# Kernel optimization log

Hardware: AMD Instinct MI355X
Metric: run time of the kernel (lower is better)

## Reference

```python
import jax, jax.numpy as jnp
import numpy as np

B, OUT, IN = 4096, 1024, 1024
BN_EPS = 1e-5


def setup_inputs() -> dict:
    key = jax.random.key(0)
    kx, k1, k2, k3 = jax.random.split(key, 4)
    # kaiming_uniform_ with a=sqrt(5): bound = sqrt(6 / ((1+a^2) * fan_in)) = 1/sqrt(fan_in)
    bound = 1.0 / np.sqrt(IN)
    x = jax.random.normal(kx, (B, IN), dtype=jnp.float32)
    c1 = jax.random.uniform(k1, (OUT, IN), jnp.float32, -bound, bound)
    c2 = jax.random.uniform(k2, (OUT, IN), jnp.float32, -bound, bound)
    c3 = jax.random.uniform(k3, (OUT, IN), jnp.float32, -bound, bound)
    bias = jnp.zeros((OUT, IN), jnp.float32)
    gamma = jnp.ones((OUT,), jnp.float32)   # BatchNorm1d weight
    beta = jnp.zeros((OUT,), jnp.float32)   # BatchNorm1d bias
    return {"x": x, "c1": c1, "c2": c2, "c3": c3, "bias": bias,
            "gamma": gamma, "beta": beta}


def reference(x, c1, c2, c3, bias, gamma, beta):
    # Fused polynomial 'matmul': out[b,o] = sum_i x*c1 + x^2*c2 + x^3*c3 + bias
    x2 = x * x
    x3 = x2 * x
    y = (jnp.einsum('bi,oi->bo', x, c1)
         + jnp.einsum('bi,oi->bo', x2, c2)
         + jnp.einsum('bi,oi->bo', x3, c3)
         + jnp.sum(bias, axis=1))  # bias reduced over in_features
    # BatchNorm1d (training mode: batch statistics, biased variance)
    mean = jnp.mean(y, axis=0)
    var = jnp.var(y, axis=0)
    return (y - mean) * jax.lax.rsqrt(var + BN_EPS) * gamma + beta
```

## Files before the change

### kernel.cpp

```cpp
#include <hip/hip_runtime.h>
#include <stdint.h>

#define B_ROWS 4096
#define OUTF   1024
#define INF    1024
#define KTOT   3072
#define BN_EPS 1e-5f
#define BM 128
#define BN 128
#define BK 64
#define NSTEP (KTOT / BK)

typedef short  short8  __attribute__((ext_vector_type(8)));
typedef float  floatx4 __attribute__((ext_vector_type(4)));

struct alignas(8) s4 { short x, y, z, w; };

#define WAIT_VM4 0x0F74
#define WAIT_VM2 0x0F72
#define WAIT_VM0 0x0F70

__device__ __forceinline__ short f2bf(float f) {
  union { float f; uint32_t u; } cv; cv.f = f;
  uint32_t u = cv.u;
  uint32_t r = (u + 0x7fffu + ((u >> 16) & 1u)) >> 16;
  return (short)r;
}

__device__ __forceinline__ void load_lds16(const void* g, void* l) {
  __builtin_amdgcn_global_load_lds(
      (const __attribute__((address_space(1))) uint32_t*)(uintptr_t)g,
      (__attribute__((address_space(3))) uint32_t*)(uint32_t)(uintptr_t)l,
      16, 0, 0);
}

__global__ void prep_all(const float4* __restrict__ x4,
                         const float4* __restrict__ c1, const float4* __restrict__ c2,
                         const float4* __restrict__ c3,
                         short* __restrict__ Xb, short* __restrict__ Wb) {
  int b = blockIdx.x;
  if (b < 4096) {
    int idx = b * 256 + threadIdx.x;
    float4 v = x4[idx];
    int row = idx >> 8;
    int c   = (idx & 255) << 2;
    size_t base = (size_t)row * KTOT + c;
    s4 p1 = { f2bf(v.x), f2bf(v.y), f2bf(v.z), f2bf(v.w) };
    float ax = v.x * v.x, ay = v.y * v.y, az = v.z * v.z, aw = v.w * v.w;
    s4 p2 = { f2bf(ax), f2bf(ay), f2bf(az), f2bf(aw) };
    s4 p3 = { f2bf(ax * v.x), f2bf(ay * v.y), f2bf(az * v.z), f2bf(aw * v.w) };
    *(s4*)&Xb[base]        = p1;
    *(s4*)&Xb[base + 1024] = p2;
    *(s4*)&Xb[base + 2048] = p3;
  } else {
    int idx = (b - 4096) * 256 + threadIdx.x;
    int row = idx >> 8;
    int c   = (idx & 255) << 2;
    size_t base = (size_t)row * KTOT + c;
    float4 a = c1[idx], bb = c2[idx], d = c3[idx];
    s4 p1 = { f2bf(a.x),  f2bf(a.y),  f2bf(a.z),  f2bf(a.w)  };
    s4 p2 = { f2bf(bb.x), f2bf(bb.y), f2bf(bb.z), f2bf(bb.w) };
    s4 p3 = { f2bf(d.x),  f2bf(d.y),  f2bf(d.z),  f2bf(d.w)  };
    *(s4*)&Wb[base]        = p1;
    *(s4*)&Wb[base + 1024] = p2;
    *(s4*)&Wb[base + 2048] = p3;
  }
}

__global__ __launch_bounds__(1024, 4) void gemm_poly(
    const short* __restrict__ Xb, const short* __restrict__ Wb,
    float* __restrict__ Y, float* __restrict__ psum, float* __restrict__ psq) {
  __shared__ __align__(16) short As[4][BM * BK];
  __shared__ __align__(16) short Bs[4][BN * BK];
  const int tid  = threadIdx.x;
  const int lane = tid & 63;
  const int wave = tid >> 6;
  const int wr = wave >> 2;
  const int wc = wave & 3;
  const int lb  = blockIdx.x;
  const int xcd = lb & 7;
  const int sl  = lb >> 3;
  const int bx  = sl & 7;
  const int by  = xcd * 4 + (sl >> 3);
  const int row0 = by * BM;
  const int col0 = bx * BN;
  const short* Ag = Xb + (size_t)row0 * KTOT;
  const short* Bg = Wb + (size_t)col0 * KTOT;
  const int frag_m = lane & 15;
  const int sel = lane >> 4;
  floatx4 acc[2][2] = {};

  const int soff = (tid >> 3) * KTOT + ((tid & 7) ^ ((tid >> 3) & 7)) * 8;
  const int ldst = tid * 8;

  #pragma unroll
  for (int t = 0; t < 3; ++t) {
    load_lds16(Ag + soff + t * BK, &As[t][ldst]);
    load_lds16(Bg + soff + t * BK, &Bs[t][ldst]);
  }

#define GSTEP(CUR, PRE, KT_PRE, DO_PRE, WAITIMM)                              \
  {                                                                           \
    __builtin_amdgcn_s_waitcnt(WAITIMM);                                      \
    __builtin_amdgcn_s_barrier();                                             \
    if (DO_PRE) {                                                             \
      load_lds16(Ag + soff + (KT_PRE), &As[PRE][ldst]);                       \
      load_lds16(Bg + soff + (KT_PRE), &Bs[PRE][ldst]);                       \
    }                                                                         \
    _Pragma("unroll")                                                         \
    for (int s = 0; s < 2; ++s) {                                             \
      short8 af[2], bfr[2];                                                   \
      _Pragma("unroll")                                                       \
      for (int i = 0; i < 2; ++i) {                                           \
        int r = wr * 32 + i * 16 + frag_m;                                    \
        int p = (s * 4 + sel) ^ (r & 7);                                      \
        af[i] = *(const short8*)&As[CUR][r * BK + p * 8];                     \
      }                                                                       \
      _Pragma("unroll")                                                       \
      for (int j = 0; j < 2; ++j) {                                           \
        int r = wc * 32 + j * 16 + frag_m;                                    \
        int p = (s * 4 + sel) ^ (r & 7);                                      \
        bfr[j] = *(const short8*)&Bs[CUR][r * BK + p * 8];                    \
      }                                                                       \
      _Pragma("unroll")                                                       \
      for (int i = 0; i < 2; ++i)                                             \
        _Pragma("unroll")                                                     \
        for (int j = 0; j < 2; ++j)                                           \
          acc[i][j] = __builtin_amdgcn_mfma_f32_16x16x32_bf16(                \
              af[i], bfr[j], acc[i][j], 0, 0, 0);                             \
    }                                                                         \
  }

  for (int t4 = 0; t4 < 44; t4 += 4) {
    GSTEP(0, 3, (t4 + 3) * BK, 1, WAIT_VM4);
    GSTEP(1, 0, (t4 + 4) * BK, 1, WAIT_VM4);
    GSTEP(2, 1, (t4 + 5) * BK, 1, WAIT_VM4);
    GSTEP(3, 2, (t4 + 6) * BK, 1, WAIT_VM4);
  }
  GSTEP(0, 3, 47 * BK, 1, WAIT_VM4);
  GSTEP(1, 0, 0, 0, WAIT_VM4);
  GSTEP(2, 0, 0, 0, WAIT_VM2);
  GSTEP(3, 0, 0, 0, WAIT_VM0);
#undef GSTEP

  float* colred = (float*)&As[0][0];
  float sv[2] = {0.f, 0.f}, sq[2] = {0.f, 0.f};
  #pragma unroll
  for (int j = 0; j < 2; ++j)
    #pragma unroll
    for (int i = 0; i < 2; ++i)
      #pragma unroll
      for (int r = 0; r < 4; ++r) {
        float v = acc[i][j][r];
        sv[j] += v; sq[j] += v * v;
      }
  #pragma unroll
  for (int j = 0; j < 2; ++j) {
    sv[j] += __shfl_xor(sv[j], 16, 64); sv[j] += __shfl_xor(sv[j], 32, 64);
    sq[j] += __shfl_xor(sq[j], 16, 64); sq[j] += __shfl_xor(sq[j], 32, 64);
  }
  if (sel == 0) {
    #pragma unroll
    for (int j = 0; j < 2; ++j) {
      int cc = wc * 32 + j * 16 + frag_m;
      colred[(wr * 2 + 0) * 128 + cc] = sv[j];
      colred[(wr * 2 + 1) * 128 + cc] = sq[j];
    }
  }
  #pragma unroll
  for (int j = 0; j < 2; ++j) {
    int gc = col0 + wc * 32 + j * 16 + frag_m;
    #pragma unroll
    for (int i = 0; i < 2; ++i) {
      int gr = row0 + wr * 32 + i * 16 + sel * 4;
      #pragma unroll
      for (int r = 0; r < 4; ++r)
        Y[(size_t)(gr + r) * OUTF + gc] = acc[i][j][r];
    }
  }
  __syncthreads();
  if (tid < BN) {
    float s0 = colred[0 * 128 + tid] + colred[2 * 128 + tid]
             + colred[4 * 128 + tid] + colred[6 * 128 + tid];
    float s1 = colred[1 * 128 + tid] + colred[3 * 128 + tid]
             + colred[5 * 128 + tid] + colred[7 * 128 + tid];
    psum[(size_t)by * OUTF + col0 + tid] = s0;
    psq [(size_t)by * OUTF + col0 + tid] = s1;
  }
}

__global__ void bn_fused(const float* __restrict__ psum, const float* __restrict__ psq,
                         const float* __restrict__ gamma, const float* __restrict__ beta,
                         float* __restrict__ Y) {
  __shared__ float sc[32], sh[32];
  const int c0 = blockIdx.x * 32;
  const int t = threadIdx.x;
  if (t < 32) {
    float s = 0.f, s2 = 0.f;
    #pragma unroll 8
    for (int p = 0; p < 32; ++p) {
      s  += psum[p * OUTF + c0 + t];
      s2 += psq [p * OUTF + c0 + t];
    }
    float mean = s * (1.0f / B_ROWS);
    float var  = s2 * (1.0f / B_ROWS) - mean * mean;
    float scale = gamma[c0 + t] * rsqrtf(var + BN_EPS);
    sc[t] = scale;
    sh[t] = beta[c0 + t] - mean * scale;
  }
  __syncthreads();
  const int f4c = t & 7;
  const int rr  = t >> 3;
  const int row0 = blockIdx.y * 256;
  float4* Y4 = (float4*)Y;
  const int cb = f4c * 4;
  float s0 = sc[cb], s1 = sc[cb+1], s2 = sc[cb+2], s3 = sc[cb+3];
  float h0 = sh[cb], h1 = sh[cb+1], h2 = sh[cb+2], h3 = sh[cb+3];
  #pragma unroll
  for (int it = 0; it < 8; ++it) {
    int row = row0 + it * 32 + rr;
    size_t idx = (size_t)row * 256 + (c0 >> 2) + f4c;
    float4 v = Y4[idx];
    v.x = v.x * s0 + h0; v.y = v.y * s1 + h1;
    v.z = v.z * s2 + h2; v.w = v.w * s3 + h3;
    Y4[idx] = v;
  }
}

extern "C" void kernel_launch(void* const* d_in, const int* in_sizes, int n_in,
                              void* d_out, int out_size, void* d_ws, size_t ws_size,
                              hipStream_t stream) {
  const float* x     = (const float*)d_in[0];
  const float* c1    = (const float*)d_in[1];
  const float* c2    = (const float*)d_in[2];
  const float* c3    = (const float*)d_in[3];
  const float* gamma = (const float*)d_in[5];
  const float* beta  = (const float*)d_in[6];
  float* out = (float*)d_out;
  char* ws = (char*)d_ws;

  short* Xb   = (short*)(ws);
  short* Wb   = (short*)(ws + 25165824);
  float* psum = (float*)(ws + 31457280);
  float* psq  = (float*)(ws + 31588352);

  prep_all<<<5120, 256, 0, stream>>>((const float4*)x, (const float4*)c1,
                                     (const float4*)c2, (const float4*)c3,
                                     Xb, Wb);

  gemm_poly<<<256, 1024, 0, stream>>>(Xb, Wb, out, psum, psq);

  dim3 bgrid(OUTF / 32, B_ROWS / 256);
  bn_fused<<<bgrid, 256, 0, stream>>>(psum, psq, gamma, beta, out);
}
```

Baseline: 123.7 us.

## Use 256-thread blocks with 64x64 per-wave tiles in polynomial GEMM

Shrinks the GEMM workgroup from 16 waves to 4 waves, so each wave now computes a 64x64 sub-tile (4x4 MFMA fragments) instead of 32x32. The intent is more register-level operand reuse per LDS fragment read and cheaper barriers. Each thread now issues four global-to-LDS loads per operand per stage, and the vmcnt wait immediates are adjusted to match. The cost is fewer waves per CU to hide latency, since only 256 blocks of 4 waves run on the device, and higher register pressure.

```diff
diff --git a/kernel.cpp b/kernel.cpp
--- a/kernel.cpp
+++ b/kernel.cpp
@@ -16,9 +16,9 @@
 
 struct alignas(8) s4 { short x, y, z, w; };
 
-#define WAIT_VM4 0x0F74
-#define WAIT_VM2 0x0F72
-#define WAIT_VM0 0x0F70
+#define WAIT_VM16 0x4F70
+#define WAIT_VM8  0x0F78
+#define WAIT_VM0  0x0F70
 
 __device__ __forceinline__ short f2bf(float f) {
   union { float f; uint32_t u; } cv; cv.f = f;
@@ -67,7 +67,7 @@
   }
 }
 
-__global__ __launch_bounds__(1024, 4) void gemm_poly(
+__global__ __launch_bounds__(256, 1) void gemm_poly(
     const short* __restrict__ Xb, const short* __restrict__ Wb,
     float* __restrict__ Y, float* __restrict__ psum, float* __restrict__ psq) {
   __shared__ __align__(16) short As[4][BM * BK];
@@ -75,8 +75,8 @@
   const int tid  = threadIdx.x;
   const int lane = tid & 63;
   const int wave = tid >> 6;
-  const int wr = wave >> 2;
-  const int wc = wave & 3;
+  const int wr = wave >> 1;
+  const int wc = wave & 1;
   const int lb  = blockIdx.x;
   const int xcd = lb & 7;
   const int sl  = lb >> 3;
@@ -88,15 +88,24 @@
   const short* Bg = Wb + (size_t)col0 * KTOT;
   const int frag_m = lane & 15;
   const int sel = lane >> 4;
-  floatx4 acc[2][2] = {};
-
-  const int soff = (tid >> 3) * KTOT + ((tid & 7) ^ ((tid >> 3) & 7)) * 8;
-  const int ldst = tid * 8;
+  floatx4 acc[4][4] = {};
+
+  int soff[4], ldst[4];
+  #pragma unroll
+  for (int q = 0; q < 4; ++q) {
+    int c = tid + q * 256;
+    soff[q] = (c >> 3) * KTOT + ((c & 7) ^ ((c >> 3) & 7)) * 8;
+    ldst[q] = c * 8;
+  }
 
   #pragma unroll
   for (int t = 0; t < 3; ++t) {
-    load_lds16(Ag + soff + t * BK, &As[t][ldst]);
-    load_lds16(Bg + soff + t * BK, &Bs[t][ldst]);
+    #pragma unroll
+    for (int q = 0; q < 4; ++q)
+      load_lds16(Ag + soff[q] + t * BK, &As[t][ldst[q]]);
+    #pragma unroll
+    for (int q = 0; q < 4; ++q)
+      load_lds16(Bg + soff[q] + t * BK, &Bs[t][ldst[q]]);
   }
 
 #define GSTEP(CUR, PRE, KT_PRE, DO_PRE, WAITIMM)                              \
@@ -104,75 +113,79 @@
     __builtin_amdgcn_s_waitcnt(WAITIMM);                                      \
     __builtin_amdgcn_s_barrier();                                             \
     if (DO_PRE) {                                                             \
-      load_lds16(Ag + soff + (KT_PRE), &As[PRE][ldst]);                       \
-      load_lds16(Bg + soff + (KT_PRE), &Bs[PRE][ldst]);                       \
+      _Pragma("unroll")                                                       \
+      for (int q = 0; q < 4; ++q)                                             \
+        load_lds16(Ag + soff[q] + (KT_PRE), &As[PRE][ldst[q]]);               \
+      _Pragma("unroll")                                                       \
+      for (int q = 0; q < 4; ++q)                                             \
+        load_lds16(Bg + soff[q] + (KT_PRE), &Bs[PRE][ldst[q]]);               \
     }                                                                         \
     _Pragma("unroll")                                                         \
     for (int s = 0; s < 2; ++s) {                                             \
-      short8 af[2], bfr[2];                                                   \
-      _Pragma("unroll")                                                       \
-      for (int i = 0; i < 2; ++i) {                                           \
-        int r = wr * 32 + i * 16 + frag_m;                                    \
+      short8 af[4], bfr[4];                                                   \
+      _Pragma("unroll")                                                       \
+      for (int i = 0; i < 4; ++i) {                                           \
+        int r = wr * 64 + i * 16 + frag_m;                                    \
         int p = (s * 4 + sel) ^ (r & 7);                                      \
         af[i] = *(const short8*)&As[CUR][r * BK + p * 8];                     \
       }                                                                       \
       _Pragma("unroll")                                                       \
-      for (int j = 0; j < 2; ++j) {                                           \
-        int r = wc * 32 + j * 16 + frag_m;                                    \
+      for (int j = 0; j < 4; ++j) {                                           \
+        int r = wc * 64 + j * 16 + frag_m;                                    \
         int p = (s * 4 + sel) ^ (r & 7);                                      \
         bfr[j] = *(const short8*)&Bs[CUR][r * BK + p * 8];                    \
       }                                                                       \
       _Pragma("unroll")                                                       \
-      for (int i = 0; i < 2; ++i)                                             \
+      for (int i = 0; i < 4; ++i)                                             \
         _Pragma("unroll")                                                     \
-        for (int j = 0; j < 2; ++j)                                           \
+        for (int j = 0; j < 4; ++j)                                           \
           acc[i][j] = __builtin_amdgcn_mfma_f32_16x16x32_bf16(                \
               af[i], bfr[j], acc[i][j], 0, 0, 0);                             \
     }                                                                         \
   }
 
   for (int t4 = 0; t4 < 44; t4 += 4) {
-    GSTEP(0, 3, (t4 + 3) * BK, 1, WAIT_VM4);
-    GSTEP(1, 0, (t4 + 4) * BK, 1, WAIT_VM4);
-    GSTEP(2, 1, (t4 + 5) * BK, 1, WAIT_VM4);
-    GSTEP(3, 2, (t4 + 6) * BK, 1, WAIT_VM4);
-  }
-  GSTEP(0, 3, 47 * BK, 1, WAIT_VM4);
-  GSTEP(1, 0, 0, 0, WAIT_VM4);
-  GSTEP(2, 0, 0, 0, WAIT_VM2);
+    GSTEP(0, 3, (t4 + 3) * BK, 1, WAIT_VM16);
+    GSTEP(1, 0, (t4 + 4) * BK, 1, WAIT_VM16);
+    GSTEP(2, 1, (t4 + 5) * BK, 1, WAIT_VM16);
+    GSTEP(3, 2, (t4 + 6) * BK, 1, WAIT_VM16);
+  }
+  GSTEP(0, 3, 47 * BK, 1, WAIT_VM16);
+  GSTEP(1, 0, 0, 0, WAIT_VM16);
+  GSTEP(2, 0, 0, 0, WAIT_VM8);
   GSTEP(3, 0, 0, 0, WAIT_VM0);
 #undef GSTEP
 
   float* colred = (float*)&As[0][0];
-  float sv[2] = {0.f, 0.f}, sq[2] = {0.f, 0.f};
-  #pragma unroll
-  for (int j = 0; j < 2; ++j)
-    #pragma unroll
-    for (int i = 0; i < 2; ++i)
+  float sv[4] = {0.f, 0.f, 0.f, 0.f}, sq[4] = {0.f, 0.f, 0.f, 0.f};
+  #pragma unroll
+  for (int j = 0; j < 4; ++j)
+    #pragma unroll
+    for (int i = 0; i < 4; ++i)
       #pragma unroll
       for (int r = 0; r < 4; ++r) {
         float v = acc[i][j][r];
         sv[j] += v; sq[j] += v * v;
       }
   #pragma unroll
-  for (int j = 0; j < 2; ++j) {
+  for (int j = 0; j < 4; ++j) {
     sv[j] += __shfl_xor(sv[j], 16, 64); sv[j] += __shfl_xor(sv[j], 32, 64);
     sq[j] += __shfl_xor(sq[j], 16, 64); sq[j] += __shfl_xor(sq[j], 32, 64);
   }
   if (sel == 0) {
     #pragma unroll
-    for (int j = 0; j < 2; ++j) {
-      int cc = wc * 32 + j * 16 + frag_m;
+    for (int j = 0; j < 4; ++j) {
+      int cc = wc * 64 + j * 16 + frag_m;
       colred[(wr * 2 + 0) * 128 + cc] = sv[j];
       colred[(wr * 2 + 1) * 128 + cc] = sq[j];
     }
   }
   #pragma unroll
-  for (int j = 0; j < 2; ++j) {
-    int gc = col0 + wc * 32 + j * 16 + frag_m;
-    #pragma unroll
-    for (int i = 0; i < 2; ++i) {
-      int gr = row0 + wr * 32 + i * 16 + sel * 4;
+  for (int j = 0; j < 4; ++j) {
+    int gc = col0 + wc * 64 + j * 16 + frag_m;
+    #pragma unroll
+    for (int i = 0; i < 4; ++i) {
+      int gr = row0 + wr * 64 + i * 16 + sel * 4;
       #pragma unroll
       for (int r = 0; r < 4; ++r)
         Y[(size_t)(gr + r) * OUTF + gc] = acc[i][j][r];
@@ -180,10 +193,8 @@
   }
   __syncthreads();
   if (tid < BN) {
-    float s0 = colred[0 * 128 + tid] + colred[2 * 128 + tid]
-             + colred[4 * 128 + tid] + colred[6 * 128 + tid];
-    float s1 = colred[1 * 128 + tid] + colred[3 * 128 + tid]
-             + colred[5 * 128 + tid] + colred[7 * 128 + tid];
+    float s0 = colred[0 * 128 + tid] + colred[2 * 128 + tid];
+    float s1 = colred[1 * 128 + tid] + colred[3 * 128 + tid];
     psum[(size_t)by * OUTF + col0 + tid] = s0;
     psq [(size_t)by * OUTF + col0 + tid] = s1;
   }
@@ -248,7 +259,7 @@
                                      (const float4*)c2, (const float4*)c3,
                                      Xb, Wb);
 
-  gemm_poly<<<256, 1024, 0, stream>>>(Xb, Wb, out, psum, psq);
+  gemm_poly<<<256, 256, 0, stream>>>(Xb, Wb, out, psum, psq);
 
   dim3 bgrid(OUTF / 32, B_ROWS / 256);
   bn_fused<<<bgrid, 256, 0, stream>>>(psum, psq, gamma, beta, out);
```

Measured after the change: 126.7 us. +2.4%, slower.

## Fuse batch-norm into GEMM epilogue via cooperative grid sync and atomics

Applied to the files above, without the earlier changes.

Removes the separate BN kernel. Each GEMM block atomically adds its column partial sums to global totals, which the prep kernel now zeroes. A cooperative grid sync follows, after which every block computes scale and shift and writes the normalized output once. This avoids writing Y and then reading and rewriting it, and drops one launch, at the cost of a grid-wide barrier and atomic contention.

```diff
diff --git a/kernel.cpp b/kernel.cpp
--- a/kernel.cpp
+++ b/kernel.cpp
@@ -1,5 +1,8 @@
 #include <hip/hip_runtime.h>
+#include <hip/hip_cooperative_groups.h>
 #include <stdint.h>
+
+namespace cg = cooperative_groups;
 
 #define B_ROWS 4096
 #define OUTF   1024
@@ -37,7 +40,8 @@
 __global__ void prep_all(const float4* __restrict__ x4,
                          const float4* __restrict__ c1, const float4* __restrict__ c2,
                          const float4* __restrict__ c3,
-                         short* __restrict__ Xb, short* __restrict__ Wb) {
+                         short* __restrict__ Xb, short* __restrict__ Wb,
+                         float* __restrict__ psz) {
   int b = blockIdx.x;
   if (b < 4096) {
     int idx = b * 256 + threadIdx.x;
@@ -52,7 +56,7 @@
     *(s4*)&Xb[base]        = p1;
     *(s4*)&Xb[base + 1024] = p2;
     *(s4*)&Xb[base + 2048] = p3;
-  } else {
+  } else if (b < 5120) {
     int idx = (b - 4096) * 256 + threadIdx.x;
     int row = idx >> 8;
     int c   = (idx & 255) << 2;
@@ -64,12 +68,17 @@
     *(s4*)&Wb[base]        = p1;
     *(s4*)&Wb[base + 1024] = p2;
     *(s4*)&Wb[base + 2048] = p3;
+  } else {
+    #pragma unroll
+    for (int k = 0; k < 8; ++k)
+      psz[threadIdx.x + k * 256] = 0.f;
   }
 }
 
 __global__ __launch_bounds__(1024, 4) void gemm_poly(
     const short* __restrict__ Xb, const short* __restrict__ Wb,
-    float* __restrict__ Y, float* __restrict__ psum, float* __restrict__ psq) {
+    float* __restrict__ Y, float* __restrict__ psumT, float* __restrict__ psqT,
+    const float* __restrict__ gamma, const float* __restrict__ beta) {
   __shared__ __align__(16) short As[4][BM * BK];
   __shared__ __align__(16) short Bs[4][BN * BK];
   const int tid  = threadIdx.x;
@@ -167,63 +176,46 @@
       colred[(wr * 2 + 1) * 128 + cc] = sq[j];
     }
   }
-  #pragma unroll
-  for (int j = 0; j < 2; ++j) {
-    int gc = col0 + wc * 32 + j * 16 + frag_m;
-    #pragma unroll
-    for (int i = 0; i < 2; ++i) {
-      int gr = row0 + wr * 32 + i * 16 + sel * 4;
-      #pragma unroll
-      for (int r = 0; r < 4; ++r)
-        Y[(size_t)(gr + r) * OUTF + gc] = acc[i][j][r];
-    }
-  }
   __syncthreads();
   if (tid < BN) {
     float s0 = colred[0 * 128 + tid] + colred[2 * 128 + tid]
              + colred[4 * 128 + tid] + colred[6 * 128 + tid];
     float s1 = colred[1 * 128 + tid] + colred[3 * 128 + tid]
              + colred[5 * 128 + tid] + colred[7 * 128 + tid];
-    psum[(size_t)by * OUTF + col0 + tid] = s0;
-    psq [(size_t)by * OUTF + col0 + tid] = s1;
-  }
-}
-
-__global__ void bn_fused(const float* __restrict__ psum, const float* __restrict__ psq,
-                         const float* __restrict__ gamma, const float* __restrict__ beta,
-                         float* __restrict__ Y) {
-  __shared__ float sc[32], sh[32];
-  const int c0 = blockIdx.x * 32;
-  const int t = threadIdx.x;
-  if (t < 32) {
-    float s = 0.f, s2 = 0.f;
-    #pragma unroll 8
-    for (int p = 0; p < 32; ++p) {
-      s  += psum[p * OUTF + c0 + t];
-      s2 += psq [p * OUTF + c0 + t];
+    atomicAdd(&psumT[col0 + tid], s0);
+    atomicAdd(&psqT [col0 + tid], s1);
+  }
+  __threadfence();
+
+  cg::this_grid().sync();
+
+  float* scaleS = (float*)&Bs[0][0];
+  float* shiftS = scaleS + 128;
+  if (tid < BN) {
+    float S  = __hip_atomic_load(&psumT[col0 + tid], __ATOMIC_RELAXED,
+                                 __HIP_MEMORY_SCOPE_AGENT);
+    float S2 = __hip_atomic_load(&psqT [col0 + tid], __ATOMIC_RELAXED,
+                                 __HIP_MEMORY_SCOPE_AGENT);
+    float mean = S * (1.0f / B_ROWS);
+    float var  = S2 * (1.0f / B_ROWS) - mean * mean;
+    float sc_  = gamma[col0 + tid] * rsqrtf(var + BN_EPS);
+    scaleS[tid] = sc_;
+    shiftS[tid] = beta[col0 + tid] - mean * sc_;
+  }
+  __syncthreads();
+  #pragma unroll
+  for (int j = 0; j < 2; ++j) {
+    int cc = wc * 32 + j * 16 + frag_m;
+    float sc_ = scaleS[cc];
+    float sh_ = shiftS[cc];
+    int gc = col0 + cc;
+    #pragma unroll
+    for (int i = 0; i < 2; ++i) {
+      int gr = row0 + wr * 32 + i * 16 + sel * 4;
+      #pragma unroll
+      for (int r = 0; r < 4; ++r)
+        Y[(size_t)(gr + r) * OUTF + gc] = acc[i][j][r] * sc_ + sh_;
     }
-    float mean = s * (1.0f / B_ROWS);
-    float var  = s2 * (1.0f / B_ROWS) - mean * mean;
-    float scale = gamma[c0 + t] * rsqrtf(var + BN_EPS);
-    sc[t] = scale;
-    sh[t] = beta[c0 + t] - mean * scale;
-  }
-  __syncthreads();
-  const int f4c = t & 7;
-  const int rr  = t >> 3;
-  const int row0 = blockIdx.y * 256;
-  float4* Y4 = (float4*)Y;
-  const int cb = f4c * 4;
-  float s0 = sc[cb], s1 = sc[cb+1], s2 = sc[cb+2], s3 = sc[cb+3];
-  float h0 = sh[cb], h1 = sh[cb+1], h2 = sh[cb+2], h3 = sh[cb+3];
-  #pragma unroll
-  for (int it = 0; it < 8; ++it) {
-    int row = row0 + it * 32 + rr;
-    size_t idx = (size_t)row * 256 + (c0 >> 2) + f4c;
-    float4 v = Y4[idx];
-    v.x = v.x * s0 + h0; v.y = v.y * s1 + h1;
-    v.z = v.z * s2 + h2; v.w = v.w * s3 + h3;
-    Y4[idx] = v;
   }
 }
 
@@ -239,17 +231,19 @@
   float* out = (float*)d_out;
   char* ws = (char*)d_ws;
 
-  short* Xb   = (short*)(ws);
-  short* Wb   = (short*)(ws + 25165824);
-  float* psum = (float*)(ws + 31457280);
-  float* psq  = (float*)(ws + 31588352);
-
-  prep_all<<<5120, 256, 0, stream>>>((const float4*)x, (const float4*)c1,
+  short* Xb    = (short*)(ws);
+  short* Wb    = (short*)(ws + 25165824);
+  float* psumT = (float*)(ws + 31457280);
+  float* psqT  = (float*)(ws + 31461376);
+
+  prep_all<<<5121, 256, 0, stream>>>((const float4*)x, (const float4*)c1,
                                      (const float4*)c2, (const float4*)c3,
-                                     Xb, Wb);
-
-  gemm_poly<<<256, 1024, 0, stream>>>(Xb, Wb, out, psum, psq);
-
-  dim3 bgrid(OUTF / 32, B_ROWS / 256);
-  bn_fused<<<bgrid, 256, 0, stream>>>(psum, psq, gamma, beta, out);
-}
+                                     Xb, Wb, psumT);
+
+  const short* XbC = Xb;
+  const short* WbC = Wb;
+  void* kargs[] = { (void*)&XbC, (void*)&WbC, (void*)&out,
+                    (void*)&psumT, (void*)&psqT,
+                    (void*)&gamma, (void*)&beta };
+  hipLaunchCooperativeKernel(gemm_poly, dim3(256), dim3(1024), kargs, 0, stream);
+}
```

After: 231.0 us. 86.7% more time.

## Fuse x power expansion and bf16 conversion into GEMM, load fp32 X tiles

Applied to the files above, without the earlier changes.

The separate prep pass that wrote x, x², x³ as bf16 into a 24MB workspace is removed. The GEMM now streams fp32 x tiles into LDS once per 64-column chunk and computes the three powers in registers, converting to bf16 before each MFMA phase. Weights are still prepacked, and the pipeline is restructured around three K-phases per x tile with a double-buffered A buffer. This cuts global traffic and one kernel's work, at the cost of extra VALU conversion inside the GEMM loop and larger fp32 LDS tiles.

```diff
diff --git a/kernel.cpp b/kernel.cpp
--- a/kernel.cpp
+++ b/kernel.cpp
@@ -1,4 +1,5 @@
 #include <hip/hip_runtime.h>
+#include <hip/hip_bf16.h>
 #include <stdint.h>
 
 #define B_ROWS 4096
@@ -9,7 +10,6 @@
 #define BM 128
 #define BN 128
 #define BK 64
-#define NSTEP (KTOT / BK)
 
 typedef short  short8  __attribute__((ext_vector_type(8)));
 typedef float  floatx4 __attribute__((ext_vector_type(4)));
@@ -18,6 +18,7 @@
 
 #define WAIT_VM4 0x0F74
 #define WAIT_VM2 0x0F72
+#define WAIT_VM1 0x0F71
 #define WAIT_VM0 0x0F70
 
 __device__ __forceinline__ short f2bf(float f) {
@@ -34,43 +35,34 @@
       16, 0, 0);
 }
 
-__global__ void prep_all(const float4* __restrict__ x4,
-                         const float4* __restrict__ c1, const float4* __restrict__ c2,
-                         const float4* __restrict__ c3,
-                         short* __restrict__ Xb, short* __restrict__ Wb) {
-  int b = blockIdx.x;
-  if (b < 4096) {
-    int idx = b * 256 + threadIdx.x;
-    float4 v = x4[idx];
-    int row = idx >> 8;
-    int c   = (idx & 255) << 2;
-    size_t base = (size_t)row * KTOT + c;
-    s4 p1 = { f2bf(v.x), f2bf(v.y), f2bf(v.z), f2bf(v.w) };
-    float ax = v.x * v.x, ay = v.y * v.y, az = v.z * v.z, aw = v.w * v.w;
-    s4 p2 = { f2bf(ax), f2bf(ay), f2bf(az), f2bf(aw) };
-    s4 p3 = { f2bf(ax * v.x), f2bf(ay * v.y), f2bf(az * v.z), f2bf(aw * v.w) };
-    *(s4*)&Xb[base]        = p1;
-    *(s4*)&Xb[base + 1024] = p2;
-    *(s4*)&Xb[base + 2048] = p3;
-  } else {
-    int idx = (b - 4096) * 256 + threadIdx.x;
-    int row = idx >> 8;
-    int c   = (idx & 255) << 2;
-    size_t base = (size_t)row * KTOT + c;
-    float4 a = c1[idx], bb = c2[idx], d = c3[idx];
-    s4 p1 = { f2bf(a.x),  f2bf(a.y),  f2bf(a.z),  f2bf(a.w)  };
-    s4 p2 = { f2bf(bb.x), f2bf(bb.y), f2bf(bb.z), f2bf(bb.w) };
-    s4 p3 = { f2bf(d.x),  f2bf(d.y),  f2bf(d.z),  f2bf(d.w)  };
-    *(s4*)&Wb[base]        = p1;
-    *(s4*)&Wb[base + 1024] = p2;
-    *(s4*)&Wb[base + 2048] = p3;
-  }
+__device__ __forceinline__ short8 cvt8(float4 a, float4 b) {
+  union { __hip_bfloat162 h[4]; short8 s; } r;
+  r.h[0] = __float22bfloat162_rn(make_float2(a.x, a.y));
+  r.h[1] = __float22bfloat162_rn(make_float2(a.z, a.w));
+  r.h[2] = __float22bfloat162_rn(make_float2(b.x, b.y));
+  r.h[3] = __float22bfloat162_rn(make_float2(b.z, b.w));
+  return r.s;
+}
+
+__global__ void prep_w(const float4* __restrict__ c1, const float4* __restrict__ c2,
+                       const float4* __restrict__ c3, short* __restrict__ Wb) {
+  int idx = blockIdx.x * 256 + threadIdx.x;
+  int row = idx >> 8;
+  int c   = (idx & 255) << 2;
+  size_t base = (size_t)row * KTOT + c;
+  float4 a = c1[idx], bb = c2[idx], d = c3[idx];
+  s4 p1 = { f2bf(a.x),  f2bf(a.y),  f2bf(a.z),  f2bf(a.w)  };
+  s4 p2 = { f2bf(bb.x), f2bf(bb.y), f2bf(bb.z), f2bf(bb.w) };
+  s4 p3 = { f2bf(d.x),  f2bf(d.y),  f2bf(d.z),  f2bf(d.w)  };
+  *(s4*)&Wb[base]        = p1;
+  *(s4*)&Wb[base + 1024] = p2;
+  *(s4*)&Wb[base + 2048] = p3;
 }
 
 __global__ __launch_bounds__(1024, 4) void gemm_poly(
-    const short* __restrict__ Xb, const short* __restrict__ Wb,
+    const float* __restrict__ X, const short* __restrict__ Wb,
     float* __restrict__ Y, float* __restrict__ psum, float* __restrict__ psq) {
-  __shared__ __align__(16) short As[4][BM * BK];
+  __shared__ __align__(16) float As32[2][BM * BK];
   __shared__ __align__(16) short Bs[4][BN * BK];
   const int tid  = threadIdx.x;
   const int lane = tid & 63;
@@ -84,43 +76,45 @@
   const int by  = xcd * 4 + (sl >> 3);
   const int row0 = by * BM;
   const int col0 = bx * BN;
-  const short* Ag = Xb + (size_t)row0 * KTOT;
+  const float* Ag = X + (size_t)row0 * INF;
   const short* Bg = Wb + (size_t)col0 * KTOT;
   const int frag_m = lane & 15;
   const int sel = lane >> 4;
   floatx4 acc[2][2] = {};
 
-  const int soff = (tid >> 3) * KTOT + ((tid & 7) ^ ((tid >> 3) & 7)) * 8;
-  const int ldst = tid * 8;
-
-  #pragma unroll
-  for (int t = 0; t < 3; ++t) {
-    load_lds16(Ag + soff + t * BK, &As[t][ldst]);
-    load_lds16(Bg + soff + t * BK, &Bs[t][ldst]);
-  }
-
-#define GSTEP(CUR, PRE, KT_PRE, DO_PRE, WAITIMM)                              \
-  {                                                                           \
-    __builtin_amdgcn_s_waitcnt(WAITIMM);                                      \
-    __builtin_amdgcn_s_barrier();                                             \
-    if (DO_PRE) {                                                             \
-      load_lds16(Ag + soff + (KT_PRE), &As[PRE][ldst]);                       \
-      load_lds16(Bg + soff + (KT_PRE), &Bs[PRE][ldst]);                       \
-    }                                                                         \
-    _Pragma("unroll")                                                         \
+  const int soffB = (tid >> 3) * KTOT + ((tid & 7) ^ ((tid >> 3) & 7)) * 8;
+  const int ldstB = tid * 8;
+  int soffA[2], ldstA[2];
+  #pragma unroll
+  for (int q = 0; q < 2; ++q) {
+    int c = tid + q * 1024;
+    int r = c >> 4, ps = c & 15;
+    soffA[q] = r * INF + (ps ^ (r & 15)) * 4;
+    ldstA[q] = c * 4;
+  }
+
+  load_lds16(Ag + soffA[0], &As32[0][ldstA[0]]);
+  load_lds16(Ag + soffA[1], &As32[0][ldstA[1]]);
+  load_lds16(Bg + soffB + 0,    &Bs[0][ldstB]);
+  load_lds16(Bg + soffB + 1024, &Bs[1][ldstB]);
+  load_lds16(Bg + soffB + 2048, &Bs[2][ldstB]);
+
+  float4 xlo[2][2], xhi[2][2];
+
+#define PHASE(BUF, POWA, POWB)                                                \
+  { _Pragma("unroll")                                                         \
     for (int s = 0; s < 2; ++s) {                                             \
       short8 af[2], bfr[2];                                                   \
       _Pragma("unroll")                                                       \
       for (int i = 0; i < 2; ++i) {                                           \
-        int r = wr * 32 + i * 16 + frag_m;                                    \
-        int p = (s * 4 + sel) ^ (r & 7);                                      \
-        af[i] = *(const short8*)&As[CUR][r * BK + p * 8];                     \
+        float4 xl = xlo[i][s], xh = xhi[i][s];                                \
+        af[i] = cvt8(POWA, POWB);                                             \
       }                                                                       \
       _Pragma("unroll")                                                       \
       for (int j = 0; j < 2; ++j) {                                           \
         int r = wc * 32 + j * 16 + frag_m;                                    \
-        int p = (s * 4 + sel) ^ (r & 7);                                      \
-        bfr[j] = *(const short8*)&Bs[CUR][r * BK + p * 8];                    \
+        int pq = (s * 4 + sel) ^ (r & 7);                                     \
+        bfr[j] = *(const short8*)&Bs[BUF][r * BK + pq * 8];                   \
       }                                                                       \
       _Pragma("unroll")                                                       \
       for (int i = 0; i < 2; ++i)                                             \
@@ -128,22 +122,63 @@
         for (int j = 0; j < 2; ++j)                                           \
           acc[i][j] = __builtin_amdgcn_mfma_f32_16x16x32_bf16(                \
               af[i], bfr[j], acc[i][j], 0, 0, 0);                             \
-    }                                                                         \
-  }
-
-  for (int t4 = 0; t4 < 44; t4 += 4) {
-    GSTEP(0, 3, (t4 + 3) * BK, 1, WAIT_VM4);
-    GSTEP(1, 0, (t4 + 4) * BK, 1, WAIT_VM4);
-    GSTEP(2, 1, (t4 + 5) * BK, 1, WAIT_VM4);
-    GSTEP(3, 2, (t4 + 6) * BK, 1, WAIT_VM4);
-  }
-  GSTEP(0, 3, 47 * BK, 1, WAIT_VM4);
-  GSTEP(1, 0, 0, 0, WAIT_VM4);
-  GSTEP(2, 0, 0, 0, WAIT_VM2);
-  GSTEP(3, 0, 0, 0, WAIT_VM0);
-#undef GSTEP
-
-  float* colred = (float*)&As[0][0];
+    } }
+
+#define READX(ACUR)                                                           \
+  { _Pragma("unroll")                                                         \
+    for (int i = 0; i < 2; ++i)                                               \
+      _Pragma("unroll")                                                       \
+      for (int s = 0; s < 2; ++s) {                                           \
+        int r = wr * 32 + i * 16 + frag_m;                                    \
+        int slt = (s * 4 + sel) * 2;                                          \
+        int q0 = slt ^ (r & 15), q1 = (slt + 1) ^ (r & 15);                   \
+        xlo[i][s] = *(const float4*)&(ACUR)[r * 64 + q0 * 4];                 \
+        xhi[i][s] = *(const float4*)&(ACUR)[r * 64 + q1 * 4];                 \
+      } }
+
+  for (int w = 0; w < 15; ++w) {
+    const int bc0 = (3 * w)     & 3;
+    const int bc1 = (3 * w + 1) & 3;
+    const int bc2 = (3 * w + 2) & 3;
+    const int bn0 = (3 * w + 3) & 3;
+    const int bn1 = (3 * w + 4) & 3;
+    const int bn2 = (3 * w + 5) & 3;
+    float* Anext = &As32[(w + 1) & 1][0];
+    const float* Acur = &As32[w & 1][0];
+    const int kA = (w + 1) * 64;
+    __builtin_amdgcn_s_waitcnt(WAIT_VM2);
+    __builtin_amdgcn_s_barrier();
+    load_lds16(Ag + soffA[0] + kA, Anext + ldstA[0]);
+    load_lds16(Ag + soffA[1] + kA, Anext + ldstA[1]);
+    load_lds16(Bg + soffB + kA, &Bs[bn0][ldstB]);
+    READX(Acur);
+    PHASE(bc0, xl, xh);
+    __builtin_amdgcn_s_waitcnt(WAIT_VM4);
+    __builtin_amdgcn_s_barrier();
+    load_lds16(Bg + soffB + 1024 + kA, &Bs[bn1][ldstB]);
+    PHASE(bc1, xl * xl, xh * xh);
+    __builtin_amdgcn_s_waitcnt(WAIT_VM4);
+    __builtin_amdgcn_s_barrier();
+    load_lds16(Bg + soffB + 2048 + kA, &Bs[bn2][ldstB]);
+    PHASE(bc2, xl * xl * xl, xh * xh * xh);
+  }
+  {
+    const float* Acur = &As32[1][0];
+    __builtin_amdgcn_s_waitcnt(WAIT_VM2);
+    __builtin_amdgcn_s_barrier();
+    READX(Acur);
+    PHASE(1, xl, xh);
+    __builtin_amdgcn_s_waitcnt(WAIT_VM1);
+    __builtin_amdgcn_s_barrier();
+    PHASE(2, xl * xl, xh * xh);
+    __builtin_amdgcn_s_waitcnt(WAIT_VM0);
+    __builtin_amdgcn_s_barrier();
+    PHASE(3, xl * xl * xl, xh * xh * xh);
+  }
+#undef PHASE
+#undef READX
+
+  float* colred = (float*)&As32[0][0];
   float sv[2] = {0.f, 0.f}, sq[2] = {0.f, 0.f};
   #pragma unroll
   for (int j = 0; j < 2; ++j)
@@ -239,16 +274,14 @@
   float* out = (float*)d_out;
   char* ws = (char*)d_ws;
 
-  short* Xb   = (short*)(ws);
-  short* Wb   = (short*)(ws + 25165824);
-  float* psum = (float*)(ws + 31457280);
-  float* psq  = (float*)(ws + 31588352);
-
-  prep_all<<<5120, 256, 0, stream>>>((const float4*)x, (const float4*)c1,
-                                     (const float4*)c2, (const float4*)c3,
-                                     Xb, Wb);
-
-  gemm_poly<<<256, 1024, 0, stream>>>(Xb, Wb, out, psum, psq);
+  short* Wb   = (short*)(ws);
+  float* psum = (float*)(ws + 6291456);
+  float* psq  = (float*)(ws + 6422528);
+
+  prep_w<<<1024, 256, 0, stream>>>((const float4*)c1, (const float4*)c2,
+                                   (const float4*)c3, Wb);
+
+  gemm_poly<<<256, 1024, 0, stream>>>(x, Wb, out, psum, psq);
 
   dim3 bgrid(OUTF / 32, B_ROWS / 256);
   bn_fused<<<bgrid, 256, 0, stream>>>(psum, psq, gamma, beta, out);
```

New measurement: 127.3 us. +2.9%, slower.
